# Performance work log

Hardware: AMD Instinct MI355X
Metric: run time of the kernel (lower is better)

Reference implementation:

```python
import jax, jax.numpy as jnp
import numpy as np

N, E, F, H, HEADS, L, G = 16384, 262144, 16, 128, 4, 5, 128
DFF = 4 * H
EPS = 1e-5

def _bn(h, g, b):
    m = h.mean(axis=0)
    v = h.var(axis=0)
    return g * (h - m) / jnp.sqrt(v + EPS) + b

def setup_inputs():
    key = jax.random.key(0)
    ks = jax.random.split(key, 20)
    rn = lambda k, s, fan: jax.random.normal(k, s, jnp.float32) / np.float32(np.sqrt(fan))
    return {
        'x': jax.random.normal(ks[0], (N, F), jnp.float32),
        'edge_index': jax.random.randint(ks[1], (2, E), 0, N),
        'batch_index': jnp.sort(jax.random.randint(ks[2], (N,), 0, G)),
        'embW': rn(ks[3], (F, H), F), 'embb': jnp.zeros((H,), jnp.float32),
        'emb_g': jnp.ones((H,), jnp.float32), 'emb_be': jnp.zeros((H,), jnp.float32),
        'Wq': rn(ks[4], (L, H, HEADS * H), H), 'bq': jnp.zeros((L, HEADS * H), jnp.float32),
        'Wk': rn(ks[5], (L, H, HEADS * H), H), 'bk': jnp.zeros((L, HEADS * H), jnp.float32),
        'Wv': rn(ks[6], (L, H, HEADS * H), H), 'bv': jnp.zeros((L, HEADS * H), jnp.float32),
        'Wskip': rn(ks[7], (L, H, H), H), 'bskip': jnp.zeros((L, H), jnp.float32),
        'Wbeta': rn(ks[8], (L, 3 * H, 1), 3 * H),
        'W1': rn(ks[9], (L, H, DFF), H), 'b1': jnp.zeros((L, DFF), jnp.float32),
        'g1': jnp.ones((L, DFF), jnp.float32), 'be1': jnp.zeros((L, DFF), jnp.float32),
        'W2': rn(ks[10], (L, DFF, H), DFF), 'b2': jnp.zeros((L, H), jnp.float32),
        'predW': rn(ks[11], (H, 1), H), 'predb': jnp.zeros((1,), jnp.float32),
    }

def reference(x, edge_index, batch_index, embW, embb, emb_g, emb_be, Wq, bq, Wk, bk, Wv, bv, Wskip, bskip, Wbeta, W1, b1, g1, be1, W2, b2, predW, predb):
    src, dst = edge_index[0], edge_index[1]
    h = jax.nn.gelu(_bn(x @ embW + embb, emb_g, emb_be), approximate=False)
    scale = jnp.float32(1.0 / np.sqrt(H))  # sqrt(out_channels) per PyG TransformerConv

    def layer(h, p):
        Wq_, bq_, Wk_, bk_, Wv_, bv_, Ws_, bs_, Wb_, W1_, b1_, g1_, be1_, W2_, b2_ = p
        q = (h @ Wq_ + bq_).reshape(N, HEADS, H)
        k = (h @ Wk_ + bk_).reshape(N, HEADS, H)
        v = (h @ Wv_ + bv_).reshape(N, HEADS, H)
        logits = jnp.einsum('ehc,ehc->eh', q[dst], k[src]) * scale  # [E, HEADS]
        m = jax.ops.segment_max(logits, dst, num_segments=N)
        p_e = jnp.exp(logits - m[dst])
        denom = jax.ops.segment_sum(p_e, dst, num_segments=N) + 1e-16
        agg = jax.ops.segment_sum(p_e[:, :, None] * v[src], dst, num_segments=N)
        out = (agg / denom[:, :, None]).mean(axis=1)  # concat=False -> mean over heads
        x_r = h @ Ws_ + bs_
        beta = jax.nn.sigmoid(jnp.concatenate([out, x_r, out - x_r], axis=-1) @ Wb_)  # [N,1]
        out = beta * x_r + (1.0 - beta) * out
        hh = jax.nn.gelu(_bn(out @ W1_ + b1_, g1_, be1_), approximate=False)
        return hh @ W2_ + b2_

    def step(carry, p):
        return layer(carry, p), None

    h, _ = jax.lax.scan(step, h, (Wq, bq, Wk, bk, Wv, bv, Wskip, bskip, Wbeta, W1, b1, g1, be1, W2, b2))
    pooled = jax.ops.segment_max(h, batch_index, num_segments=G)  # MaxAggregation
    return (pooled @ predW + predb).reshape(-1)
```

## Files before the change

kernel.cpp:

```cpp
#include <hip/hip_runtime.h>
#include <hip/hip_bf16.h>

using bf16 = __hip_bfloat16;
typedef __attribute__((ext_vector_type(8))) short bf16x8;
typedef __attribute__((ext_vector_type(4))) float f32x4;

constexpr int N_   = 16384;
constexpr int E_   = 262144;
constexpr int F_   = 16;
constexpr int H_   = 128;
constexpr int NF2_ = 1152;
constexpr int DFF_ = 512;
constexpr int G_   = 128;
constexpr int L_   = 5;
constexpr float EPS_ = 1e-5f;

constexpr int WCAT2SZ = NF2_ * 128;
constexpr int W1TSZ   = 512 * 128;
constexpr int W2TSZ   = 512 * 128;
constexpr int TRBLKS  = 5 * 208;

__device__ __forceinline__ float gelu_f(float x) {
  return 0.5f * x * (1.0f + erff(x * 0.70710678118654752440f));
}

__device__ __forceinline__ void unpack8(const uint4 w, float* f) {
  f[0] = __uint_as_float(w.x << 16); f[1] = __uint_as_float(w.x & 0xFFFF0000u);
  f[2] = __uint_as_float(w.y << 16); f[3] = __uint_as_float(w.y & 0xFFFF0000u);
  f[4] = __uint_as_float(w.z << 16); f[5] = __uint_as_float(w.z & 0xFFFF0000u);
  f[6] = __uint_as_float(w.w << 16); f[7] = __uint_as_float(w.w & 0xFFFF0000u);
}

__global__ __launch_bounds__(256) void k_ptrans(
    const float* __restrict__ Wv, const float* __restrict__ Ws,
    const float* __restrict__ W1, const float* __restrict__ W2,
    const float* __restrict__ bv, const float* __restrict__ bs,
    bf16* __restrict__ Wcat2, bf16* __restrict__ W1t, bf16* __restrict__ W2t,
    float* __restrict__ bcat) {
  __shared__ float lds[32][33];
  const int b = blockIdx.x;
  if (b >= TRBLKS) {
    int j = (b - TRBLKS) * 256 + threadIdx.x;
    if (j < 5 * NF2_) {
      int l = j / NF2_, c = j % NF2_;
      if (c >= 512)
        bcat[j] = (c < 1024) ? bv[l * 512 + (c - 512)] : bs[l * 128 + (c - 1024)];
    }
    return;
  }
  const int l = b / 208, t = b % 208;
  const float* src; int C; bf16* dst; int dld; int nof; int tt;
  if (t < 64) {
    tt = t;
    src = Wv + (size_t)l * 128 * 512; C = 512;
    dst = Wcat2 + (size_t)l * WCAT2SZ; dld = 128; nof = 512;
  } else if (t < 80) {
    tt = t - 64;
    src = Ws + (size_t)l * 128 * 128; C = 128;
    dst = Wcat2 + (size_t)l * WCAT2SZ; dld = 128; nof = 1024;
  } else if (t < 144) {
    tt = t - 80;
    src = W1 + (size_t)l * 128 * 512; C = 512;
    dst = W1t + (size_t)l * W1TSZ; dld = 128; nof = 0;
  } else {
    tt = t - 144;
    src = W2 + (size_t)l * 512 * 128; C = 128;
    dst = W2t + (size_t)l * W2TSZ; dld = 512; nof = 0;
  }
  const int tpr = C >> 5;
  const int r0 = (tt / tpr) * 32, c0 = (tt % tpr) * 32;
  const int j = threadIdx.x & 31, g = threadIdx.x >> 5;
#pragma unroll
  for (int ii = 0; ii < 4; ++ii) {
    int i = g * 4 + ii;
    lds[i][j] = src[(size_t)(r0 + i) * C + c0 + j];
  }
  __syncthreads();
#pragma unroll
  for (int ii = 0; ii < 4; ++ii) {
    int i = g * 4 + ii;
    dst[(size_t)(nof + c0 + i) * dld + r0 + j] = __float2bfloat16(lds[j][i]);
  }
}

__global__ __launch_bounds__(256) void k_gmat(
    const float* __restrict__ Wq, const float* __restrict__ Wk,
    const float* __restrict__ bq,
    bf16* __restrict__ Wcat2, float* __restrict__ bcat) {
  __shared__ float lq[32][132];
  __shared__ float lk[32][132];
  const int l = blockIdx.x >> 2, h = blockIdx.x & 3;
  const int half = blockIdx.y;
  const int tid = threadIdx.x;
  const int c = tid & 127, ch = tid >> 7;
  const int cp0 = half * 64 + ch * 32;
  const float* wqL = Wq + (size_t)l * 128 * 512 + h * 128;
  const float* wkL = Wk + (size_t)l * 128 * 512 + h * 128;
  float acc[32];
#pragma unroll
  for (int j = 0; j < 32; ++j) acc[j] = 0.f;
  for (int a0 = 0; a0 < 128; a0 += 32) {
    __syncthreads();
#pragma unroll
    for (int q4 = 0; q4 < 4; ++q4) {
      int f4 = tid * 4 + q4;
      int row = f4 >> 3, af = f4 & 7;
      float4 gq = *reinterpret_cast<const float4*>(wqL + (size_t)row * 512 + a0 + af * 4);
      float4 gk = *reinterpret_cast<const float4*>(wkL + (size_t)row * 512 + a0 + af * 4);
      lq[af * 4 + 0][row] = gq.x; lq[af * 4 + 1][row] = gq.y;
      lq[af * 4 + 2][row] = gq.z; lq[af * 4 + 3][row] = gq.w;
      lk[af * 4 + 0][row] = gk.x; lk[af * 4 + 1][row] = gk.y;
      lk[af * 4 + 2][row] = gk.z; lk[af * 4 + 3][row] = gk.w;
    }
    __syncthreads();
    for (int a = 0; a < 32; ++a) {
      float wq = lq[a][c];
#pragma unroll
      for (int j = 0; j < 32; ++j) acc[j] = fmaf(wq, lk[a][cp0 + j], acc[j]);
    }
  }
  bf16* gt = Wcat2 + (size_t)l * WCAT2SZ;
#pragma unroll
  for (int j = 0; j < 32; ++j)
    gt[(size_t)(h * 128 + cp0 + j) * 128 + c] = __float2bfloat16(acc[j]);
  if (half == 0 && ch == 0) {
    float s = 0.f;
    const float* wkr = wkL + (size_t)c * 512;
    const float* bqh = bq + (size_t)l * 512 + h * 128;
    for (int a = 0; a < 128; ++a) s = fmaf(wkr[a], bqh[a], s);
    bcat[(size_t)l * NF2_ + h * 128 + c] = s;
  }
}

__global__ __launch_bounds__(256) void k_embed2(const float* __restrict__ x,
    const float* __restrict__ W, const float* __restrict__ b,
    float* __restrict__ out, float* __restrict__ ss, float* __restrict__ sq) {
  __shared__ float xs[128][16];
  __shared__ float wsm[16][128];
  __shared__ float sr[2][128], qr[2][128];
  const int blk = blockIdx.x;
  const int t = threadIdx.x;
  for (int i = t; i < 16 * 128; i += 256) wsm[i >> 7][i & 127] = W[i];
  for (int i = t; i < 128 * 16; i += 256) xs[i >> 4][i & 15] = x[(size_t)blk * 2048 + i];
  __syncthreads();
  const int c = t & 127, rg = t >> 7;
  float bc = b[c];
  float s = 0.f, q = 0.f;
  for (int r = rg * 64; r < rg * 64 + 64; ++r) {
    float v = bc;
#pragma unroll
    for (int f = 0; f < 16; ++f) v = fmaf(xs[r][f], wsm[f][c], v);
    out[(size_t)(blk * 128 + r) * 128 + c] = v;
    s += v; q += v * v;
  }
  sr[rg][c] = s; qr[rg][c] = q;
  __syncthreads();
  if (t < 128) { ss[blk * 128 + t] = sr[0][t] + sr[1][t]; sq[blk * 128 + t] = qr[0][t] + qr[1][t]; }
}

template<int NC>
__global__ void k_bn_finalize(const float* __restrict__ sums, const float* __restrict__ sumsq,
                              const float* __restrict__ g, const float* __restrict__ be,
                              float* __restrict__ a, float* __restrict__ cc) {
  int c = blockIdx.x * 128 + threadIdx.x;
  if (c >= NC) return;
  float s = 0.f, q = 0.f;
  for (int b = 0; b < 128; ++b) { s += sums[b * NC + c]; q += sumsq[b * NC + c]; }
  float mean = s * (1.0f / N_);
  float var  = q * (1.0f / N_) - mean * mean;
  float inv  = rsqrtf(var + EPS_);
  float aa   = g[c] * inv;
  a[c]  = aa;
  cc[c] = be[c] - aa * mean;
}

template<int NC>
__global__ void k_bn_apply_gelu_cast(const float* __restrict__ xin, const float* __restrict__ a,
                                     const float* __restrict__ cc, bf16* __restrict__ outb) {
  int i4 = (blockIdx.x * 256 + threadIdx.x) * 4;
  int c = i4 & (NC - 1);
  float4 v = *reinterpret_cast<const float4*>(xin + i4);
  union { uint2 u2; bf16 h[4]; } pk;
  pk.h[0] = __float2bfloat16(gelu_f(fmaf(a[c + 0], v.x, cc[c + 0])));
  pk.h[1] = __float2bfloat16(gelu_f(fmaf(a[c + 1], v.y, cc[c + 1])));
  pk.h[2] = __float2bfloat16(gelu_f(fmaf(a[c + 2], v.z, cc[c + 2])));
  pk.h[3] = __float2bfloat16(gelu_f(fmaf(a[c + 3], v.w, cc[c + 3])));
  *reinterpret_cast<uint2*>(outb + i4) = pk.u2;
}

__global__ void k_count(const int* __restrict__ dst, int* __restrict__ deg) {
  int e = blockIdx.x * 256 + threadIdx.x;
  if (e < E_) atomicAdd(&deg[dst[e]], 1);
}

__global__ void k_bsum(const int* __restrict__ deg, int* __restrict__ bsum) {
  __shared__ int sh[256];
  int t = threadIdx.x;
  sh[t] = deg[blockIdx.x * 256 + t];
  __syncthreads();
  for (int d = 128; d > 0; d >>= 1) { if (t < d) sh[t] += sh[t + d]; __syncthreads(); }
  if (t == 0) bsum[blockIdx.x] = sh[0];
}

__global__ void k_boffs(const int* __restrict__ deg, const int* __restrict__ bsum,
                        int* __restrict__ offs) {
  __shared__ int sh[256];
  __shared__ int baseSh;
  int t = threadIdx.x;
  if (t < 64) {
    int v = bsum[t];
    int s = v;
    for (int d = 1; d < 64; d <<= 1) { int o = __shfl_up(s, d); if (t >= d) s += o; }
    if (t == (int)blockIdx.x) baseSh = s - v;
  }
  int v = deg[blockIdx.x * 256 + t];
  sh[t] = v;
  __syncthreads();
  for (int d = 1; d < 256; d <<= 1) {
    int add = (t >= d) ? sh[t - d] : 0;
    __syncthreads();
    sh[t] += add;
    __syncthreads();
  }
  offs[blockIdx.x * 256 + t] = baseSh + sh[t] - v;
  if (blockIdx.x == 63 && t == 255) offs[N_] = E_;
}

__global__ void k_scatter(const int* __restrict__ src, const int* __restrict__ dst,
                          const int* __restrict__ off, int* __restrict__ cursor,
                          int* __restrict__ srcs) {
  int e = blockIdx.x * 256 + threadIdx.x;
  if (e < E_) {
    int d = dst[e];
    int pos = off[d] + atomicAdd(&cursor[d], 1);
    srcs[pos] = src[e];
  }
}

template<int KDIM, int NOUT, int TM, int MODE>
__global__ __launch_bounds__(256) void k_mfma(
    const bf16* __restrict__ A, const float* __restrict__ Af,
    const bf16* __restrict__ BT, const float* __restrict__ bias,
    float* __restrict__ outF, bf16* __restrict__ outB,
    float* __restrict__ zfp, bf16* __restrict__ Vpp, float* __restrict__ xrp,
    float* __restrict__ ss, float* __restrict__ sq,
    const float* __restrict__ aCol, const float* __restrict__ cCol) {
  constexpr int MF = TM / 32;
  __shared__ bf16 As[TM][72];
  __shared__ bf16 Bs[128][72];
  __shared__ float sred[2][128], qred[2][128];
  __shared__ float aS[MODE == 4 ? KDIM : 1], cS[MODE == 4 ? KDIM : 1];
  const int tid = threadIdx.x;
  const int wid = tid >> 6, lane = tid & 63;
  const int wr = wid >> 1, wc = wid & 1;
  const int m0 = blockIdx.x * TM, n0 = blockIdx.y * 128;
  const int ln = lane & 15, lq = lane >> 4;
  if constexpr (MODE == 4) {
    for (int i = tid; i < KDIM; i += 256) { aS[i] = aCol[i]; cS[i] = cCol[i]; }
    __syncthreads();
  }
  f32x4 acc[MF][4];
#pragma unroll
  for (int i = 0; i < MF; ++i)
#pragma unroll
    for (int j = 0; j < 4; ++j) acc[i][j] = (f32x4){0.f, 0.f, 0.f, 0.f};

  for (int k0 = 0; k0 < KDIM; k0 += 64) {
#pragma unroll
    for (int u = tid; u < TM * 8; u += 256) {
      int r = u >> 3, c = u & 7;
      if constexpr (MODE == 4) {
        const float4* ap = reinterpret_cast<const float4*>(Af + (size_t)(m0 + r) * KDIM + k0 + c * 8);
        float4 f0 = ap[0], f1 = ap[1];
        float f[8] = {f0.x, f0.y, f0.z, f0.w, f1.x, f1.y, f1.z, f1.w};
        int colb = k0 + c * 8;
        union { uint4 u4; bf16 h[8]; } pk;
#pragma unroll
        for (int j = 0; j < 8; ++j)
          pk.h[j] = __float2bfloat16(gelu_f(fmaf(aS[colb + j], f[j], cS[colb + j])));
        *(uint4*)(&As[r][c * 8]) = pk.u4;
      } else {
        *(uint4*)(&As[r][c * 8]) = *(const uint4*)(A + (size_t)(m0 + r) * KDIM + k0 + c * 8);
      }
    }
#pragma unroll
    for (int u = tid; u < 1024; u += 256) {
      int r = u >> 3, c = u & 7;
      *(uint4*)(&Bs[r][c * 8]) = *(const uint4*)(BT + (size_t)(n0 + r) * KDIM + k0 + c * 8);
    }
    __syncthreads();
#pragma unroll
    for (int kk = 0; kk < 2; ++kk) {
      bf16x8 af[MF], bg[4];
#pragma unroll
      for (int i = 0; i < MF; ++i)
        af[i] = *(const bf16x8*)(&As[wr * (TM / 2) + i * 16 + ln][kk * 32 + lq * 8]);
#pragma unroll
      for (int j = 0; j < 4; ++j)
        bg[j] = *(const bf16x8*)(&Bs[wc * 64 + j * 16 + ln][kk * 32 + lq * 8]);
#pragma unroll
      for (int i = 0; i < MF; ++i)
#pragma unroll
        for (int j = 0; j < 4; ++j)
          acc[i][j] = __builtin_amdgcn_mfma_f32_16x16x32_bf16(af[i], bg[j], acc[i][j], 0, 0, 0);
    }
    __syncthreads();
  }
  float ssj[4] = {0.f, 0.f, 0.f, 0.f}, sqj[4] = {0.f, 0.f, 0.f, 0.f};
#pragma unroll
  for (int i = 0; i < MF; ++i) {
#pragma unroll
    for (int j = 0; j < 4; ++j) {
      int gcol = n0 + wc * 64 + j * 16 + ln;
      float bv = bias[gcol];
      int row0 = m0 + wr * (TM / 2) + i * 16 + lq * 4;
#pragma unroll
      for (int qq = 0; qq < 4; ++qq) {
        float val = acc[i][j][qq] + bv;
        int row = row0 + qq;
        if (MODE == 3) {
          outF[(size_t)row * NOUT + gcol] = val;
          ssj[j] += val; sqj[j] += val * val;
        } else if (MODE == 4) {
          outF[(size_t)row * NOUT + gcol] = val;
          outB[(size_t)row * NOUT + gcol] = __float2bfloat16(val);
        } else {
          if (n0 < 512)       zfp[(size_t)row * 512 + gcol] = val;
          else if (n0 < 1024) Vpp[(size_t)row * 512 + (gcol - 512)] = __float2bfloat16(val);
          else                xrp[(size_t)row * H_ + (gcol - 1024)] = val;
        }
      }
    }
  }
  if constexpr (MODE == 3) {
#pragma unroll
    for (int j = 0; j < 4; ++j) {
      ssj[j] += __shfl_xor(ssj[j], 16); ssj[j] += __shfl_xor(ssj[j], 32);
      sqj[j] += __shfl_xor(sqj[j], 16); sqj[j] += __shfl_xor(sqj[j], 32);
    }
    if (lq == 0) {
#pragma unroll
      for (int j = 0; j < 4; ++j) {
        sred[wr][wc * 64 + j * 16 + ln] = ssj[j];
        qred[wr][wc * 64 + j * 16 + ln] = sqj[j];
      }
    }
    __syncthreads();
    if (tid < 128) {
      ss[(size_t)blockIdx.x * NOUT + n0 + tid] = sred[0][tid] + sred[1][tid];
      sq[(size_t)blockIdx.x * NOUT + n0 + tid] = qred[0][tid] + qred[1][tid];
    }
  }
}

__global__ __launch_bounds__(256) void k_attn(const float* __restrict__ zf,
    const bf16* __restrict__ hb, const bf16* __restrict__ Vp,
    const float* __restrict__ xr, const float* __restrict__ Wb,
    const int* __restrict__ srcs, const int* __restrict__ off,
    bf16* __restrict__ gated) {
  const int wave = threadIdx.x >> 6;
  const int lane = threadIdx.x & 63;
  const int bid = blockIdx.x;
  const int swz = ((bid & 7) << 9) | (bid >> 3);
  const int node = swz * 4 + wave;
  const int sub = lane & 15;
  const float scale = 0.08838834764831845f;
  float qf[8];
  {
    const float4* qp = reinterpret_cast<const float4*>(zf + (size_t)node * 512) + lane * 2;
    float4 a = qp[0], b = qp[1];
    qf[0]=a.x; qf[1]=a.y; qf[2]=a.z; qf[3]=a.w;
    qf[4]=b.x; qf[5]=b.y; qf[6]=b.z; qf[7]=b.w;
  }
  float m = -1e30f, den = 0.f;
  float acc[8] = {0.f, 0.f, 0.f, 0.f, 0.f, 0.f, 0.f, 0.f};
  const int s0 = off[node], s1 = off[node + 1];
  if (s0 < s1) {
    int i0 = srcs[s0];
    int i1 = (s0 + 1 < s1) ? srcs[s0 + 1] : i0;
    uint4 h0 = *(const uint4*)(hb + (size_t)i0 * 128 + sub * 8);
    uint4 v0 = *(const uint4*)(Vp + (size_t)i0 * 512 + lane * 8);
    uint4 h1 = *(const uint4*)(hb + (size_t)i1 * 128 + sub * 8);
    uint4 v1 = *(const uint4*)(Vp + (size_t)i1 * 512 + lane * 8);
    for (int t = s0; t < s1; t += 2) {
      int j0 = (t + 2 < s1) ? srcs[t + 2] : i0;
      int j1 = (t + 3 < s1) ? srcs[t + 3] : i0;
      uint4 nh0 = *(const uint4*)(hb + (size_t)j0 * 128 + sub * 8);
      uint4 nv0 = *(const uint4*)(Vp + (size_t)j0 * 512 + lane * 8);
      uint4 nh1 = *(const uint4*)(hb + (size_t)j1 * 128 + sub * 8);
      uint4 nv1 = *(const uint4*)(Vp + (size_t)j1 * 512 + lane * 8);
      {
        float hf[8]; unpack8(h0, hf);
        float p = hf[0]*qf[0]+hf[1]*qf[1]+hf[2]*qf[2]+hf[3]*qf[3]
                + hf[4]*qf[4]+hf[5]*qf[5]+hf[6]*qf[6]+hf[7]*qf[7];
        p += __shfl_xor(p, 1); p += __shfl_xor(p, 2);
        p += __shfl_xor(p, 4); p += __shfl_xor(p, 8);
        float logit = p * scale;
        if (logit > m + 8.f) {
          float co = __expf(m - logit);
          den *= co;
#pragma unroll
          for (int j = 0; j < 8; ++j) acc[j] *= co;
          m = logit;
        }
        float pe = __expf(logit - m);
        den += pe;
        float vf[8]; unpack8(v0, vf);
#pragma unroll
        for (int j = 0; j < 8; ++j) acc[j] = fmaf(pe, vf[j], acc[j]);
      }
      if (t + 1 < s1) {
        float hf[8]; unpack8(h1, hf);
        float p = hf[0]*qf[0]+hf[1]*qf[1]+hf[2]*qf[2]+hf[3]*qf[3]
                + hf[4]*qf[4]+hf[5]*qf[5]+hf[6]*qf[6]+hf[7]*qf[7];
        p += __shfl_xor(p, 1); p += __shfl_xor(p, 2);
        p += __shfl_xor(p, 4); p += __shfl_xor(p, 8);
        float logit = p * scale;
        if (logit > m + 8.f) {
          float co = __expf(m - logit);
          den *= co;
#pragma unroll
          for (int j = 0; j < 8; ++j) acc[j] *= co;
          m = logit;
        }
        float pe = __expf(logit - m);
        den += pe;
        float vf[8]; unpack8(v1, vf);
#pragma unroll
        for (int j = 0; j < 8; ++j) acc[j] = fmaf(pe, vf[j], acc[j]);
      }
      h0 = nh0; v0 = nv0; h1 = nh1; v1 = nv1;
    }
  }
  float inv = 1.f / (den + 1e-16f);
  float r[8];
#pragma unroll
  for (int j = 0; j < 8; ++j) {
    r[j] = acc[j] * inv;
    r[j] += __shfl_xor(r[j], 16);
    r[j] += __shfl_xor(r[j], 32);
    r[j] *= 0.25f;
  }
  const int c0 = sub * 8;
  float xv[8];
  const float* xp = xr + (size_t)node * H_ + c0;
#pragma unroll
  for (int j = 0; j < 8; ++j) xv[j] = xp[j];
  float s = 0.f;
#pragma unroll
  for (int j = 0; j < 8; ++j) {
    int c = c0 + j;
    s += r[j] * (Wb[c] + Wb[256 + c]) + xv[j] * (Wb[128 + c] - Wb[256 + c]);
  }
  s += __shfl_xor(s, 1); s += __shfl_xor(s, 2);
  s += __shfl_xor(s, 4); s += __shfl_xor(s, 8);
  float beta = 1.f / (1.f + __expf(-s));
  if (lane < 16) {
    union { uint4 u4; bf16 h[8]; } pk;
#pragma unroll
    for (int j = 0; j < 8; ++j) pk.h[j] = __float2bfloat16(beta * xv[j] + (1.f - beta) * r[j]);
    *reinterpret_cast<uint4*>(gated + (size_t)node * H_ + c0) = pk.u4;
  }
}

__global__ __launch_bounds__(256) void k_poolpred(const float* __restrict__ h,
    const int* __restrict__ batch, const float* __restrict__ predW,
    const float* __restrict__ predb, float* __restrict__ out) {
  __shared__ float cm[2][128];
  __shared__ int range[2];
  const int g = blockIdx.x, t = threadIdx.x;
  if (t < 2) {
    int target = g + t;
    int lo = 0, hi = N_;
    while (lo < hi) { int mid = (lo + hi) >> 1; if (batch[mid] < target) lo = mid + 1; else hi = mid; }
    range[t] = lo;
  }
  __syncthreads();
  const int lo = range[0], hi = range[1];
  const int c = t & 127, rg = t >> 7;
  float m = -3.402823466e+38f;
  for (int r = lo + rg; r < hi; r += 2) m = fmaxf(m, h[(size_t)r * H_ + c]);
  cm[rg][c] = m;
  __syncthreads();
  if (t < 64) {
    float m0 = fmaxf(cm[0][t], cm[1][t]);
    float m1 = fmaxf(cm[0][t + 64], cm[1][t + 64]);
    float s = m0 * predW[t] + m1 * predW[t + 64];
#pragma unroll
    for (int d = 1; d < 64; d <<= 1) s += __shfl_xor(s, d);
    if (t == 0) out[g] = s + predb[0];
  }
}

extern "C" void kernel_launch(void* const* d_in, const int* in_sizes, int n_in,
                              void* d_out, int out_size, void* d_ws, size_t ws_size,
                              hipStream_t stream) {
  const float* x      = (const float*)d_in[0];
  const int*   edge   = (const int*)d_in[1];
  const int*   esrc   = edge;
  const int*   edst   = edge + E_;
  const int*   batch  = (const int*)d_in[2];
  const float* embW   = (const float*)d_in[3];
  const float* embb   = (const float*)d_in[4];
  const float* emb_g  = (const float*)d_in[5];
  const float* emb_be = (const float*)d_in[6];
  const float* Wq     = (const float*)d_in[7];
  const float* bq     = (const float*)d_in[8];
  const float* Wk     = (const float*)d_in[9];
  const float* bk     = (const float*)d_in[10];
  const float* Wv     = (const float*)d_in[11];
  const float* bv     = (const float*)d_in[12];
  const float* Wskip  = (const float*)d_in[13];
  const float* bskip  = (const float*)d_in[14];
  const float* Wbeta  = (const float*)d_in[15];
  const float* W1     = (const float*)d_in[16];
  const float* b1     = (const float*)d_in[17];
  const float* g1     = (const float*)d_in[18];
  const float* be1    = (const float*)d_in[19];
  const float* W2     = (const float*)d_in[20];
  const float* b2     = (const float*)d_in[21];
  const float* predW  = (const float*)d_in[22];
  const float* predb  = (const float*)d_in[23];
  (void)bk;

  float* ws = (float*)d_ws;
  size_t o = 0;
  auto alloc_f = [&](size_t n) { float* p = ws + o; o += n; return p; };
  float* h32   = alloc_f((size_t)N_ * H_);
  float* t1    = alloc_f((size_t)N_ * DFF_);
  float* xr    = alloc_f((size_t)N_ * H_);
  float* zf    = alloc_f((size_t)N_ * 512);
  float* stats = alloc_f(2 * 128 * DFF_);
  float* a_c   = alloc_f(DFF_);
  float* c_c   = alloc_f(DFF_);
  float* bcat  = alloc_f(5 * NF2_);
  bf16* bp = (bf16*)(ws + o);
  size_t ob = 0;
  auto alloc_b = [&](size_t n) { bf16* p = bp + ob; ob += n; return p; };
  bf16* Vp   = alloc_b((size_t)N_ * 512);
  bf16* hb   = alloc_b((size_t)N_ * H_);
  bf16* gated= alloc_b((size_t)N_ * H_);
  bf16* Wcat2= alloc_b((size_t)5 * WCAT2SZ);
  bf16* W1t  = alloc_b((size_t)5 * W1TSZ);
  bf16* W2t  = alloc_b((size_t)5 * W2TSZ);
  int* deg    = (int*)(bp + ob);
  int* offs   = deg + N_;
  int* cursor = offs + N_ + 1;
  int* srcs   = cursor + N_;
  int* bsum   = srcs + E_;

  k_ptrans<<<TRBLKS + (5 * NF2_ + 255) / 256, 256, 0, stream>>>(
      Wv, Wskip, W1, W2, bv, bskip, Wcat2, W1t, W2t, bcat);
  k_gmat<<<dim3(20, 2), 256, 0, stream>>>(Wq, Wk, bq, Wcat2, bcat);

  hipMemsetAsync(deg, 0, N_ * sizeof(int), stream);
  hipMemsetAsync(cursor, 0, N_ * sizeof(int), stream);
  k_count  <<<E_ / 256, 256, 0, stream>>>(edst, deg);
  k_bsum   <<<64, 256, 0, stream>>>(deg, bsum);
  k_boffs  <<<64, 256, 0, stream>>>(deg, bsum, offs);
  k_scatter<<<E_ / 256, 256, 0, stream>>>(esrc, edst, offs, cursor, srcs);

  k_embed2<<<128, 256, 0, stream>>>(x, embW, embb, t1, stats, stats + 128 * 128);
  k_bn_finalize<128><<<1, 128, 0, stream>>>(stats, stats + 128 * 128, emb_g, emb_be, a_c, c_c);
  k_bn_apply_gelu_cast<128><<<N_ * H_ / 1024, 256, 0, stream>>>(t1, a_c, c_c, hb);

  for (int l = 0; l < L_; ++l) {
    const float* Wb_ = Wbeta + (size_t)l * 3 * H_;
    const float* b1_ = b1 + (size_t)l * DFF_;
    const float* g1_ = g1 + (size_t)l * DFF_;
    const float* be1_= be1 + (size_t)l * DFF_;
    const float* b2_ = b2 + (size_t)l * H_;

    k_mfma<128, NF2_, 128, 2><<<dim3(N_ / 128, NF2_ / 128), 256, 0, stream>>>(
        hb, nullptr, Wcat2 + (size_t)l * WCAT2SZ, bcat + (size_t)l * NF2_,
        nullptr, nullptr, zf, Vp, xr, nullptr, nullptr, nullptr, nullptr);

    k_attn<<<N_ / 4, 256, 0, stream>>>(zf, hb, Vp, xr, Wb_, srcs, offs, gated);

    k_mfma<128, 512, 128, 3><<<dim3(N_ / 128, 4), 256, 0, stream>>>(
        gated, nullptr, W1t + (size_t)l * W1TSZ, b1_, t1, nullptr, nullptr, nullptr, nullptr,
        stats, stats + 128 * 512, nullptr, nullptr);

    k_bn_finalize<512><<<4, 128, 0, stream>>>(stats, stats + 128 * 512, g1_, be1_, a_c, c_c);

    k_mfma<512, 128, 64, 4><<<dim3(N_ / 64, 1), 256, 0, stream>>>(
        nullptr, t1, W2t + (size_t)l * W2TSZ, b2_, h32, hb, nullptr, nullptr, nullptr,
        nullptr, nullptr, a_c, c_c);
  }

  k_poolpred<<<G_, 256, 0, stream>>>(h32, batch, predW, predb, (float*)d_out);
}
```

Before: 793.3 us.

## Aggregate raw h per head and apply Wv after attention

The V projection is no longer computed per node before attention. Attention now aggregates the bf16 h rows with softmax weights per head into a 512-wide buffer, then one GEMM with a stacked, quarter-scaled Wv produces the head-mean output. The bias mean is added only for nodes with incoming edges, and the beta gate moves into a separate kernel. This shrinks the first GEMM and cuts the per-edge gather from 1 KB of V to 256 B of h, at the cost of an extra GEMM, an extra kernel launch and a 512-wide bf16 intermediate write.

```diff
diff --git a/kernel.cpp b/kernel.cpp
--- a/kernel.cpp
+++ b/kernel.cpp
@@ -9,16 +9,17 @@
 constexpr int E_   = 262144;
 constexpr int F_   = 16;
 constexpr int H_   = 128;
-constexpr int NF2_ = 1152;
+constexpr int NF1_ = 640;
 constexpr int DFF_ = 512;
 constexpr int G_   = 128;
 constexpr int L_   = 5;
 constexpr float EPS_ = 1e-5f;
 
-constexpr int WCAT2SZ = NF2_ * 128;
+constexpr int WCAT1SZ = NF1_ * 128;
 constexpr int W1TSZ   = 512 * 128;
 constexpr int W2TSZ   = 512 * 128;
-constexpr int TRBLKS  = 5 * 208;
+constexpr int WVSSZ   = 128 * 512;
+constexpr int TRBLKS  = 5 * 144;
 
 __device__ __forceinline__ float gelu_f(float x) {
   return 0.5f * x * (1.0f + erff(x * 0.70710678118654752440f));
@@ -32,38 +33,38 @@
 }
 
 __global__ __launch_bounds__(256) void k_ptrans(
-    const float* __restrict__ Wv, const float* __restrict__ Ws,
-    const float* __restrict__ W1, const float* __restrict__ W2,
-    const float* __restrict__ bv, const float* __restrict__ bs,
-    bf16* __restrict__ Wcat2, bf16* __restrict__ W1t, bf16* __restrict__ W2t,
-    float* __restrict__ bcat) {
+    const float* __restrict__ Ws, const float* __restrict__ W1,
+    const float* __restrict__ W2, const float* __restrict__ bs,
+    const float* __restrict__ bv,
+    bf16* __restrict__ Wcat1, bf16* __restrict__ W1t, bf16* __restrict__ W2t,
+    float* __restrict__ bcat, float* __restrict__ bvm) {
   __shared__ float lds[32][33];
   const int b = blockIdx.x;
   if (b >= TRBLKS) {
     int j = (b - TRBLKS) * 256 + threadIdx.x;
-    if (j < 5 * NF2_) {
-      int l = j / NF2_, c = j % NF2_;
-      if (c >= 512)
-        bcat[j] = (c < 1024) ? bv[l * 512 + (c - 512)] : bs[l * 128 + (c - 1024)];
+    if (j < 5 * NF1_) {
+      int l = j / NF1_, c = j % NF1_;
+      if (c >= 512) bcat[j] = bs[l * 128 + (c - 512)];
+    } else if (j < 5 * NF1_ + 5 * 128) {
+      int j2 = j - 5 * NF1_;
+      int l = j2 / 128, n = j2 % 128;
+      bvm[j2] = 0.25f * (bv[l * 512 + n] + bv[l * 512 + 128 + n]
+                       + bv[l * 512 + 256 + n] + bv[l * 512 + 384 + n]);
     }
     return;
   }
-  const int l = b / 208, t = b % 208;
+  const int l = b / 144, t = b % 144;
   const float* src; int C; bf16* dst; int dld; int nof; int tt;
-  if (t < 64) {
+  if (t < 16) {
     tt = t;
-    src = Wv + (size_t)l * 128 * 512; C = 512;
-    dst = Wcat2 + (size_t)l * WCAT2SZ; dld = 128; nof = 512;
+    src = Ws + (size_t)l * 128 * 128; C = 128;
+    dst = Wcat1 + (size_t)l * WCAT1SZ; dld = 128; nof = 512;
   } else if (t < 80) {
-    tt = t - 64;
-    src = Ws + (size_t)l * 128 * 128; C = 128;
-    dst = Wcat2 + (size_t)l * WCAT2SZ; dld = 128; nof = 1024;
-  } else if (t < 144) {
-    tt = t - 80;
+    tt = t - 16;
     src = W1 + (size_t)l * 128 * 512; C = 512;
     dst = W1t + (size_t)l * W1TSZ; dld = 128; nof = 0;
   } else {
-    tt = t - 144;
+    tt = t - 80;
     src = W2 + (size_t)l * 512 * 128; C = 128;
     dst = W2t + (size_t)l * W2TSZ; dld = 512; nof = 0;
   }
@@ -83,10 +84,33 @@
   }
 }
 
+__global__ __launch_bounds__(256) void k_wvprep(const float* __restrict__ Wv,
+                                                bf16* __restrict__ Wvs) {
+  __shared__ float lds[32][33];
+  const int b = blockIdx.x;
+  const int l = b / 64, rest = b % 64;
+  const int h = rest / 16, tt = rest % 16;
+  const int r0 = (tt / 4) * 32, c0 = (tt % 4) * 32;
+  const float* src = Wv + (size_t)l * 128 * 512 + h * 128;
+  bf16* dst = Wvs + (size_t)l * WVSSZ;
+  const int j = threadIdx.x & 31, g = threadIdx.x >> 5;
+#pragma unroll
+  for (int ii = 0; ii < 4; ++ii) {
+    int i = g * 4 + ii;
+    lds[i][j] = src[(size_t)(r0 + i) * 512 + c0 + j];
+  }
+  __syncthreads();
+#pragma unroll
+  for (int ii = 0; ii < 4; ++ii) {
+    int i = g * 4 + ii;
+    dst[(size_t)(c0 + i) * 512 + h * 128 + r0 + j] = __float2bfloat16(0.25f * lds[j][i]);
+  }
+}
+
 __global__ __launch_bounds__(256) void k_gmat(
     const float* __restrict__ Wq, const float* __restrict__ Wk,
     const float* __restrict__ bq,
-    bf16* __restrict__ Wcat2, float* __restrict__ bcat) {
+    bf16* __restrict__ Wcat1, float* __restrict__ bcat) {
   __shared__ float lq[32][132];
   __shared__ float lk[32][132];
   const int l = blockIdx.x >> 2, h = blockIdx.x & 3;
@@ -119,7 +143,7 @@
       for (int j = 0; j < 32; ++j) acc[j] = fmaf(wq, lk[a][cp0 + j], acc[j]);
     }
   }
-  bf16* gt = Wcat2 + (size_t)l * WCAT2SZ;
+  bf16* gt = Wcat1 + (size_t)l * WCAT1SZ;
 #pragma unroll
   for (int j = 0; j < 32; ++j)
     gt[(size_t)(h * 128 + cp0 + j) * 128 + c] = __float2bfloat16(acc[j]);
@@ -128,7 +152,7 @@
     const float* wkr = wkL + (size_t)c * 512;
     const float* bqh = bq + (size_t)l * 512 + h * 128;
     for (int a = 0; a < 128; ++a) s = fmaf(wkr[a], bqh[a], s);
-    bcat[(size_t)l * NF2_ + h * 128 + c] = s;
+    bcat[(size_t)l * NF1_ + h * 128 + c] = s;
   }
 }
 
@@ -242,7 +266,7 @@
     const bf16* __restrict__ A, const float* __restrict__ Af,
     const bf16* __restrict__ BT, const float* __restrict__ bias,
     float* __restrict__ outF, bf16* __restrict__ outB,
-    float* __restrict__ zfp, bf16* __restrict__ Vpp, float* __restrict__ xrp,
+    float* __restrict__ zfp, float* __restrict__ xrp,
     float* __restrict__ ss, float* __restrict__ sq,
     const float* __restrict__ aCol, const float* __restrict__ cCol) {
   constexpr int MF = TM / 32;
@@ -312,7 +336,8 @@
 #pragma unroll
     for (int j = 0; j < 4; ++j) {
       int gcol = n0 + wc * 64 + j * 16 + ln;
-      float bv = bias[gcol];
+      float bv = 0.f;
+      if constexpr (MODE != 5) bv = bias[gcol];
       int row0 = m0 + wr * (TM / 2) + i * 16 + lq * 4;
 #pragma unroll
       for (int qq = 0; qq < 4; ++qq) {
@@ -324,10 +349,11 @@
         } else if (MODE == 4) {
           outF[(size_t)row * NOUT + gcol] = val;
           outB[(size_t)row * NOUT + gcol] = __float2bfloat16(val);
+        } else if (MODE == 5) {
+          outF[(size_t)row * NOUT + gcol] = val;
         } else {
-          if (n0 < 512)       zfp[(size_t)row * 512 + gcol] = val;
-          else if (n0 < 1024) Vpp[(size_t)row * 512 + (gcol - 512)] = __float2bfloat16(val);
-          else                xrp[(size_t)row * H_ + (gcol - 1024)] = val;
+          if (n0 < 512) zfp[(size_t)row * 512 + gcol] = val;
+          else          xrp[(size_t)row * H_ + (gcol - 512)] = val;
         }
       }
     }
@@ -354,10 +380,8 @@
 }
 
 __global__ __launch_bounds__(256) void k_attn(const float* __restrict__ zf,
-    const bf16* __restrict__ hb, const bf16* __restrict__ Vp,
-    const float* __restrict__ xr, const float* __restrict__ Wb,
-    const int* __restrict__ srcs, const int* __restrict__ off,
-    bf16* __restrict__ gated) {
+    const bf16* __restrict__ hb, const int* __restrict__ srcs,
+    const int* __restrict__ off, bf16* __restrict__ aggB) {
   const int wave = threadIdx.x >> 6;
   const int lane = threadIdx.x & 63;
   const int bid = blockIdx.x;
@@ -379,16 +403,12 @@
     int i0 = srcs[s0];
     int i1 = (s0 + 1 < s1) ? srcs[s0 + 1] : i0;
     uint4 h0 = *(const uint4*)(hb + (size_t)i0 * 128 + sub * 8);
-    uint4 v0 = *(const uint4*)(Vp + (size_t)i0 * 512 + lane * 8);
     uint4 h1 = *(const uint4*)(hb + (size_t)i1 * 128 + sub * 8);
-    uint4 v1 = *(const uint4*)(Vp + (size_t)i1 * 512 + lane * 8);
     for (int t = s0; t < s1; t += 2) {
       int j0 = (t + 2 < s1) ? srcs[t + 2] : i0;
       int j1 = (t + 3 < s1) ? srcs[t + 3] : i0;
       uint4 nh0 = *(const uint4*)(hb + (size_t)j0 * 128 + sub * 8);
-      uint4 nv0 = *(const uint4*)(Vp + (size_t)j0 * 512 + lane * 8);
       uint4 nh1 = *(const uint4*)(hb + (size_t)j1 * 128 + sub * 8);
-      uint4 nv1 = *(const uint4*)(Vp + (size_t)j1 * 512 + lane * 8);
       {
         float hf[8]; unpack8(h0, hf);
         float p = hf[0]*qf[0]+hf[1]*qf[1]+hf[2]*qf[2]+hf[3]*qf[3]
@@ -405,9 +425,8 @@
         }
         float pe = __expf(logit - m);
         den += pe;
-        float vf[8]; unpack8(v0, vf);
-#pragma unroll
-        for (int j = 0; j < 8; ++j) acc[j] = fmaf(pe, vf[j], acc[j]);
+#pragma unroll
+        for (int j = 0; j < 8; ++j) acc[j] = fmaf(pe, hf[j], acc[j]);
       }
       if (t + 1 < s1) {
         float hf[8]; unpack8(h1, hf);
@@ -425,42 +444,40 @@
         }
         float pe = __expf(logit - m);
         den += pe;
-        float vf[8]; unpack8(v1, vf);
-#pragma unroll
-        for (int j = 0; j < 8; ++j) acc[j] = fmaf(pe, vf[j], acc[j]);
+#pragma unroll
+        for (int j = 0; j < 8; ++j) acc[j] = fmaf(pe, hf[j], acc[j]);
       }
-      h0 = nh0; v0 = nv0; h1 = nh1; v1 = nv1;
+      h0 = nh0; h1 = nh1;
     }
   }
   float inv = 1.f / (den + 1e-16f);
-  float r[8];
-#pragma unroll
-  for (int j = 0; j < 8; ++j) {
-    r[j] = acc[j] * inv;
-    r[j] += __shfl_xor(r[j], 16);
-    r[j] += __shfl_xor(r[j], 32);
-    r[j] *= 0.25f;
-  }
-  const int c0 = sub * 8;
-  float xv[8];
-  const float* xp = xr + (size_t)node * H_ + c0;
-#pragma unroll
-  for (int j = 0; j < 8; ++j) xv[j] = xp[j];
-  float s = 0.f;
-#pragma unroll
-  for (int j = 0; j < 8; ++j) {
-    int c = c0 + j;
-    s += r[j] * (Wb[c] + Wb[256 + c]) + xv[j] * (Wb[128 + c] - Wb[256 + c]);
-  }
-  s += __shfl_xor(s, 1); s += __shfl_xor(s, 2);
-  s += __shfl_xor(s, 4); s += __shfl_xor(s, 8);
+  union { uint4 u4; bf16 h[8]; } pk;
+#pragma unroll
+  for (int j = 0; j < 8; ++j) pk.h[j] = __float2bfloat16(acc[j] * inv);
+  *reinterpret_cast<uint4*>(aggB + (size_t)node * 512 + lane * 8) = pk.u4;
+}
+
+__global__ __launch_bounds__(256) void k_beta(const float* __restrict__ out0,
+    const float* __restrict__ xr, const float* __restrict__ Wb,
+    const float* __restrict__ bvm, const int* __restrict__ off,
+    bf16* __restrict__ gated) {
+  const int wave = threadIdx.x >> 6;
+  const int lane = threadIdx.x & 63;
+  const int node = blockIdx.x * 4 + wave;
+  const int c0 = lane * 2;
+  bool hasE = off[node + 1] > off[node];
+  float2 o = *reinterpret_cast<const float2*>(out0 + (size_t)node * H_ + c0);
+  if (hasE) { o.x += bvm[c0]; o.y += bvm[c0 + 1]; }
+  float2 xv = *reinterpret_cast<const float2*>(xr + (size_t)node * H_ + c0);
+  float s = o.x * (Wb[c0] + Wb[256 + c0]) + xv.x * (Wb[128 + c0] - Wb[256 + c0])
+          + o.y * (Wb[c0 + 1] + Wb[256 + c0 + 1]) + xv.y * (Wb[128 + c0 + 1] - Wb[256 + c0 + 1]);
+#pragma unroll
+  for (int d = 1; d < 64; d <<= 1) s += __shfl_xor(s, d);
   float beta = 1.f / (1.f + __expf(-s));
-  if (lane < 16) {
-    union { uint4 u4; bf16 h[8]; } pk;
-#pragma unroll
-    for (int j = 0; j < 8; ++j) pk.h[j] = __float2bfloat16(beta * xv[j] + (1.f - beta) * r[j]);
-    *reinterpret_cast<uint4*>(gated + (size_t)node * H_ + c0) = pk.u4;
-  }
+  union { unsigned u; bf16 h[2]; } pk;
+  pk.h[0] = __float2bfloat16(beta * xv.x + (1.f - beta) * o.x);
+  pk.h[1] = __float2bfloat16(beta * xv.y + (1.f - beta) * o.y);
+  *reinterpret_cast<unsigned*>(gated + (size_t)node * H_ + c0) = pk.u;
 }
 
 __global__ __launch_bounds__(256) void k_poolpred(const float* __restrict__ h,
@@ -507,7 +524,6 @@
   const float* Wq     = (const float*)d_in[7];
   const float* bq     = (const float*)d_in[8];
   const float* Wk     = (const float*)d_in[9];
-  const float* bk     = (const float*)d_in[10];
   const float* Wv     = (const float*)d_in[11];
   const float* bv     = (const float*)d_in[12];
   const float* Wskip  = (const float*)d_in[13];
@@ -521,37 +537,41 @@
   const float* b2     = (const float*)d_in[21];
   const float* predW  = (const float*)d_in[22];
   const float* predb  = (const float*)d_in[23];
-  (void)bk;
 
   float* ws = (float*)d_ws;
   size_t o = 0;
   auto alloc_f = [&](size_t n) { float* p = ws + o; o += n; return p; };
-  float* h32   = alloc_f((size_t)N_ * H_);
-  float* t1    = alloc_f((size_t)N_ * DFF_);
+  float* A32   = alloc_f((size_t)N_ * 512);
+  float* B32   = alloc_f((size_t)N_ * H_);
   float* xr    = alloc_f((size_t)N_ * H_);
-  float* zf    = alloc_f((size_t)N_ * 512);
   float* stats = alloc_f(2 * 128 * DFF_);
   float* a_c   = alloc_f(DFF_);
   float* c_c   = alloc_f(DFF_);
-  float* bcat  = alloc_f(5 * NF2_);
+  float* bcat  = alloc_f(5 * NF1_);
+  float* bvm   = alloc_f(5 * 128);
   bf16* bp = (bf16*)(ws + o);
   size_t ob = 0;
   auto alloc_b = [&](size_t n) { bf16* p = bp + ob; ob += n; return p; };
-  bf16* Vp   = alloc_b((size_t)N_ * 512);
+  bf16* aggB = alloc_b((size_t)N_ * 512);
   bf16* hb   = alloc_b((size_t)N_ * H_);
   bf16* gated= alloc_b((size_t)N_ * H_);
-  bf16* Wcat2= alloc_b((size_t)5 * WCAT2SZ);
+  bf16* Wcat1= alloc_b((size_t)5 * WCAT1SZ);
   bf16* W1t  = alloc_b((size_t)5 * W1TSZ);
   bf16* W2t  = alloc_b((size_t)5 * W2TSZ);
+  bf16* Wvs  = alloc_b((size_t)5 * WVSSZ);
   int* deg    = (int*)(bp + ob);
   int* offs   = deg + N_;
   int* cursor = offs + N_ + 1;
   int* srcs   = cursor + N_;
   int* bsum   = srcs + E_;
 
-  k_ptrans<<<TRBLKS + (5 * NF2_ + 255) / 256, 256, 0, stream>>>(
-      Wv, Wskip, W1, W2, bv, bskip, Wcat2, W1t, W2t, bcat);
-  k_gmat<<<dim3(20, 2), 256, 0, stream>>>(Wq, Wk, bq, Wcat2, bcat);
+  float* zf   = A32;  float* t1 = A32;
+  float* out0 = B32;  float* h32 = B32;
+
+  k_ptrans<<<TRBLKS + 15, 256, 0, stream>>>(Wskip, W1, W2, bskip, bv,
+                                            Wcat1, W1t, W2t, bcat, bvm);
+  k_wvprep<<<320, 256, 0, stream>>>(Wv, Wvs);
+  k_gmat<<<dim3(20, 2), 256, 0, stream>>>(Wq, Wk, bq, Wcat1, bcat);
 
   hipMemsetAsync(deg, 0, N_ * sizeof(int), stream);
   hipMemsetAsync(cursor, 0, N_ * sizeof(int), stream);
@@ -560,9 +580,9 @@
   k_boffs  <<<64, 256, 0, stream>>>(deg, bsum, offs);
   k_scatter<<<E_ / 256, 256, 0, stream>>>(esrc, edst, offs, cursor, srcs);
 
-  k_embed2<<<128, 256, 0, stream>>>(x, embW, embb, t1, stats, stats + 128 * 128);
+  k_embed2<<<128, 256, 0, stream>>>(x, embW, embb, A32, stats, stats + 128 * 128);
   k_bn_finalize<128><<<1, 128, 0, stream>>>(stats, stats + 128 * 128, emb_g, emb_be, a_c, c_c);
-  k_bn_apply_gelu_cast<128><<<N_ * H_ / 1024, 256, 0, stream>>>(t1, a_c, c_c, hb);
+  k_bn_apply_gelu_cast<128><<<N_ * H_ / 1024, 256, 0, stream>>>(A32, a_c, c_c, hb);
 
   for (int l = 0; l < L_; ++l) {
     const float* Wb_ = Wbeta + (size_t)l * 3 * H_;
@@ -571,20 +591,26 @@
     const float* be1_= be1 + (size_t)l * DFF_;
     const float* b2_ = b2 + (size_t)l * H_;
 
-    k_mfma<128, NF2_, 128, 2><<<dim3(N_ / 128, NF2_ / 128), 256, 0, stream>>>(
-        hb, nullptr, Wcat2 + (size_t)l * WCAT2SZ, bcat + (size_t)l * NF2_,
-        nullptr, nullptr, zf, Vp, xr, nullptr, nullptr, nullptr, nullptr);
-
-    k_attn<<<N_ / 4, 256, 0, stream>>>(zf, hb, Vp, xr, Wb_, srcs, offs, gated);
+    k_mfma<128, NF1_, 128, 2><<<dim3(N_ / 128, NF1_ / 128), 256, 0, stream>>>(
+        hb, nullptr, Wcat1 + (size_t)l * WCAT1SZ, bcat + (size_t)l * NF1_,
+        nullptr, nullptr, zf, xr, nullptr, nullptr, nullptr, nullptr);
+
+    k_attn<<<N_ / 4, 256, 0, stream>>>(zf, hb, srcs, offs, aggB);
+
+    k_mfma<512, 128, 64, 5><<<dim3(N_ / 64, 1), 256, 0, stream>>>(
+        aggB, nullptr, Wvs + (size_t)l * WVSSZ, nullptr,
+        out0, nullptr, nullptr, nullptr, nullptr, nullptr, nullptr, nullptr);
+
+    k_beta<<<N_ / 4, 256, 0, stream>>>(out0, xr, Wb_, bvm + (size_t)l * 128, offs, gated);
 
     k_mfma<128, 512, 128, 3><<<dim3(N_ / 128, 4), 256, 0, stream>>>(
-        gated, nullptr, W1t + (size_t)l * W1TSZ, b1_, t1, nullptr, nullptr, nullptr, nullptr,
+        gated, nullptr, W1t + (size_t)l * W1TSZ, b1_, t1, nullptr, nullptr, nullptr,
         stats, stats + 128 * 512, nullptr, nullptr);
 
     k_bn_finalize<512><<<4, 128, 0, stream>>>(stats, stats + 128 * 512, g1_, be1_, a_c, c_c);
 
     k_mfma<512, 128, 64, 4><<<dim3(N_ / 64, 1), 256, 0, stream>>>(
-        nullptr, t1, W2t + (size_t)l * W2TSZ, b2_, h32, hb, nullptr, nullptr, nullptr,
+        nullptr, t1, W2t + (size_t)l * W2TSZ, b2_, h32, hb, nullptr, nullptr,
         nullptr, nullptr, a_c, c_c);
   }
 
```

New measurement: 765.8 us. 3.5% less time.
